# Kernel optimization log

Hardware: AMD Instinct MI355X
Metric: run time of the kernel (lower is better)

Reference implementation:

```python
import jax, jax.numpy as jnp
import numpy as np

ROPE_BASE = 10000.0

def rope_2d(x, h, w):
    # x: (b, h, w, c); 2D RoPE, first half of pair-channels rotated by row angle, second by col angle
    b, _, _, c = x.shape
    k_max = c // 4  # c // (2 * num_spatial_dims)
    theta = 1.0 / (ROPE_BASE ** (jnp.arange(k_max, dtype=jnp.float32) / k_max))  # (k_max,)
    ang_h = jnp.arange(h, dtype=jnp.float32)[:, None] * theta  # (h, k_max)
    ang_w = jnp.arange(w, dtype=jnp.float32)[:, None] * theta  # (w, k_max)
    # angles: (h, w, 2*k_max) = cat([i*theta, j*theta], -1)
    angles = jnp.concatenate([
        jnp.broadcast_to(ang_h[:, None, :], (h, w, k_max)),
        jnp.broadcast_to(ang_w[None, :, :], (h, w, k_max)),
    ], axis=-1)
    cos = jnp.cos(angles)  # (h, w, c//2)
    sin = jnp.sin(angles)
    xr = x[..., 0::2]  # consecutive-pair real parts (b,h,w,c//2)
    xi = x[..., 1::2]
    out_r = xr * cos - xi * sin
    out_i = xr * sin + xi * cos
    return jnp.stack([out_r, out_i], axis=-1).reshape(b, h, w, c)

def linear_attention_fwd(x, h, w, qk_w, qk_b, lepe_w, lepe_b, num_heads=4):
    b, n, c = x.shape
    head_dim = c // num_heads
    qk = x @ qk_w.T + qk_b  # (b, n, 2c)
    q, k = qk[..., :c], qk[..., c:]
    v = x
    q = jax.nn.elu(q) + 1.0
    k = jax.nn.elu(k) + 1.0
    q_rope = rope_2d(q.reshape(b, h, w, c), h, w).reshape(b, n, num_heads, head_dim).transpose(0, 2, 1, 3)
    k_rope = rope_2d(k.reshape(b, h, w, c), h, w).reshape(b, n, num_heads, head_dim).transpose(0, 2, 1, 3)
    qh = q.reshape(b, n, num_heads, head_dim).transpose(0, 2, 1, 3)  # (b,H,n,d)
    kh = k.reshape(b, n, num_heads, head_dim).transpose(0, 2, 1, 3)
    vh = v.reshape(b, n, num_heads, head_dim).transpose(0, 2, 1, 3)
    k_mean = kh.mean(axis=2)  # (b,H,d)
    z = 1.0 / (jnp.einsum('bhnd,bhd->bhn', qh, k_mean) + 1e-6)  # (b,H,n)
    inv_n = 1.0 / n
    kv = jnp.einsum('bhnd,bhne->bhde', k_rope, vh) * inv_n  # (b,H,d,d)
    out = jnp.einsum('bhnd,bhde->bhne', q_rope, kv) * z[..., None]  # (b,H,n,d)
    out = out.transpose(0, 2, 1, 3).reshape(b, n, c)
    # LePE: depthwise 3x3 conv on v in NCHW
    v_img = v.reshape(b, h, w, c).transpose(0, 3, 1, 2)  # (b,c,h,w)
    lepe = jax.lax.conv_general_dilated(
        v_img, lepe_w, window_strides=(1, 1), padding='SAME',
        feature_group_count=c, dimension_numbers=('NCHW', 'OIHW', 'NCHW'))
    lepe = lepe + lepe_b[None, :, None, None]
    out = out + lepe.transpose(0, 2, 3, 1).reshape(b, n, c)
    return out.transpose(0, 2, 1).reshape(b, c, h, w)

def setup_inputs() -> dict:
    key = jax.random.key(0)
    ks = jax.random.split(key, 5)
    b, h, w, c = 16, 128, 128, 64
    n = h * w
    x = jax.random.normal(ks[0], (b, n, c), dtype=jnp.float32)
    qk_w = jax.random.normal(ks[1], (2 * c, c), dtype=jnp.float32) * (1.0 / np.sqrt(c))
    qk_b = jax.random.normal(ks[2], (2 * c,), dtype=jnp.float32) * 0.02
    lepe_w = jax.random.normal(ks[3], (c, 1, 3, 3), dtype=jnp.float32) * (1.0 / 3.0)
    lepe_b = jax.random.normal(ks[4], (c,), dtype=jnp.float32) * 0.02
    return {"x": x, "h": h, "w": w, "qk_w": qk_w, "qk_b": qk_b, "lepe_w": lepe_w, "lepe_b": lepe_b}

def reference(x, h, w, qk_w, qk_b, lepe_w, lepe_b):
    return linear_attention_fwd(x, h, w, qk_w, qk_b, lepe_w, lepe_b, num_heads=4)
```

## Files before the change

kernel.cpp:

```cpp
#include <hip/hip_runtime.h>

#define B_   16
#define C_   64
#define HH   128
#define WW   128
#define NN   (HH*WW)
#define PADB 72
#define PADO 66

typedef short short8 __attribute__((ext_vector_type(8)));
typedef float f32x4  __attribute__((ext_vector_type(4)));

#define NEG_L2_10K_OVER16 (-0.8304820237218406f)

__device__ __forceinline__ float act_elu1(float v) {
    return v > 0.f ? v + 1.f : __expf(v);
}
__device__ __forceinline__ short f2bf(float f) {
    union { float f; unsigned u; } v; v.f = f;
    unsigned r = (v.u + 0x7FFFu + ((v.u >> 16) & 1u)) >> 16;
    return (short)r;
}
__device__ __forceinline__ unsigned cvt2bf(float lo, float hi) {
    unsigned r;
    asm("v_cvt_pk_bf16_f32 %0, %1, %2" : "=v"(r) : "v"(lo), "v"(hi));
    return r;
}

__device__ __forceinline__ void p1_chunk(
    const float* __restrict__ xb, int n0, int xbase, const short8 bk[2][4],
    const float* biasK, const float* sy, const float* cy, const float* th,
    int w, int ln, int quad, short* sKTb, float* kmacc)
{
    short8 aF[2];
    #pragma unroll
    for (int ks = 0; ks < 2; ++ks) {
        const float* ap = xb + (size_t)(n0 + 16*w + ln)*C_ + 32*ks + 8*quad;
        float4 a0 = *(const float4*)ap, a1 = *(const float4*)(ap + 4);
        union { unsigned u[4]; short8 s; } af;
        af.u[0] = cvt2bf(a0.x, a0.y); af.u[1] = cvt2bf(a0.z, a0.w);
        af.u[2] = cvt2bf(a1.x, a1.y); af.u[3] = cvt2bf(a1.z, a1.w);
        aF[ks] = af.s;
    }
    f32x4 ak[4];
    #pragma unroll
    for (int nt = 0; nt < 4; ++nt) ak[nt] = (f32x4){0.f,0.f,0.f,0.f};
    #pragma unroll
    for (int ks = 0; ks < 2; ++ks)
        #pragma unroll
        for (int nt = 0; nt < 4; ++nt)
            ak[nt] = __builtin_amdgcn_mfma_f32_16x16x32_bf16(aF[ks], bk[ks][nt], ak[nt], 0, 0, 0);
    const int p_base = 16*w + 4*quad;
    #pragma unroll
    for (int nt = 0; nt < 4; ++nt) {
        const int j = 16*nt + ln;
        const float sgn = (j & 1) ? 1.f : -1.f;
        #pragma unroll
        for (int r = 0; r < 4; ++r) {
            int p_loc = p_base + r;
            float kval = act_elu1(ak[nt][r] + biasK[nt]);
            kmacc[nt] += kval;
            float P = __shfl_xor(kval, 1);
            float s, c;
            if (nt < 2) { s = sy[nt]; c = cy[nt]; }
            else __sincosf((float)(xbase + p_loc) * th[nt & 1], &s, &c);
            sKTb[j*PADB + p_loc] = f2bf(kval*c + sgn*P*s);
        }
    }
}

__device__ __forceinline__ void p1_kv(
    const short* sKTb, const short* sXTb, int w, int ln, int quad, f32x4* acc2)
{
    #pragma unroll
    for (int ks = 0; ks < 2; ++ks) {
        short8 a  = *(const short8*)(sKTb + (16*w + ln)*PADB + 32*ks + 8*quad);
        short8 bf = *(const short8*)(sXTb + (16*w + ln)*PADB + 32*ks + 8*quad);
        *acc2 = __builtin_amdgcn_mfma_f32_16x16x32_bf16(a, bf, *acc2, 0, 0, 0);
    }
}

__global__ __launch_bounds__(256, 4) void la_phase1(
    const float* __restrict__ x, const float* __restrict__ qk_w,
    const float* __restrict__ qk_b, float* __restrict__ g_kv,
    float* __restrict__ g_km)
{
    __shared__ __align__(16) char pool[4*64*PADB*2 + 256*4];
    short* sXT0 = (short*)pool;
    short* sKT0 = sXT0 + 64*PADB;
    short* sXT1 = sKT0 + 64*PADB;
    short* sKT1 = sXT1 + 64*PADB;
    float* kmp  = (float*)(sKT1 + 64*PADB);

    const int tid  = threadIdx.x;
    const int w    = tid >> 6;
    const int ln   = tid & 15;
    const int quad = (tid >> 4) & 3;
    const int b    = blockIdx.y;
    const int bx   = blockIdx.x;
    const int nblk = ((bx & 7) << 4) | (bx >> 3);
    const float* xb = x + (size_t)b * (size_t)(NN * C_);

    short8 bk[2][4];
    #pragma unroll
    for (int ks = 0; ks < 2; ++ks)
        #pragma unroll
        for (int nt = 0; nt < 4; ++nt) {
            const float* wp = qk_w + (64 + 16*nt + ln)*C_ + 32*ks + 8*quad;
            float4 w0 = *(const float4*)wp, w1 = *(const float4*)(wp + 4);
            union { unsigned u[4]; short8 s; } uf;
            uf.u[0] = cvt2bf(w0.x, w0.y); uf.u[1] = cvt2bf(w0.z, w0.w);
            uf.u[2] = cvt2bf(w1.x, w1.y); uf.u[3] = cvt2bf(w1.z, w1.w);
            bk[ks][nt] = uf.s;
        }
    float biasK[4];
    #pragma unroll
    for (int nt = 0; nt < 4; ++nt) biasK[nt] = qk_b[64 + 16*nt + ln];

    float th[2];
    #pragma unroll
    for (int i = 0; i < 2; ++i)
        th[i] = exp2f(NEG_L2_10K_OVER16 * (float)(8*i + (ln >> 1)));
    float sy[2], cy[2];
    #pragma unroll
    for (int i = 0; i < 2; ++i) __sincosf((float)nblk * th[i], &sy[i], &cy[i]);

    const int srow = tid & 63, scol = (tid >> 6) << 2;
    float4 xv0[4], xv1[4];
    #pragma unroll
    for (int it = 0; it < 4; ++it)
        xv0[it] = *(const float4*)(xb + (size_t)(nblk*128 + srow)*C_ + scol + 16*it);
    #pragma unroll
    for (int it = 0; it < 4; ++it) {
        int k4 = scol + 16*it;
        unsigned p01 = cvt2bf(xv0[it].x, xv0[it].y), p23 = cvt2bf(xv0[it].z, xv0[it].w);
        sXT0[(k4+0)*PADB + srow] = (short)p01;
        sXT0[(k4+1)*PADB + srow] = (short)(p01 >> 16);
        sXT0[(k4+2)*PADB + srow] = (short)p23;
        sXT0[(k4+3)*PADB + srow] = (short)(p23 >> 16);
    }
    #pragma unroll
    for (int it = 0; it < 4; ++it)
        xv1[it] = *(const float4*)(xb + (size_t)(nblk*128 + 64 + srow)*C_ + scol + 16*it);
    __syncthreads();

    f32x4 acc2 = {0.f, 0.f, 0.f, 0.f};
    float kmacc[4] = {0.f, 0.f, 0.f, 0.f};

    p1_chunk(xb, nblk*128, 0, bk, biasK, sy, cy, th, w, ln, quad, sKT0, kmacc);
    #pragma unroll
    for (int it = 0; it < 4; ++it) {
        int k4 = scol + 16*it;
        unsigned p01 = cvt2bf(xv1[it].x, xv1[it].y), p23 = cvt2bf(xv1[it].z, xv1[it].w);
        sXT1[(k4+0)*PADB + srow] = (short)p01;
        sXT1[(k4+1)*PADB + srow] = (short)(p01 >> 16);
        sXT1[(k4+2)*PADB + srow] = (short)p23;
        sXT1[(k4+3)*PADB + srow] = (short)(p23 >> 16);
    }
    __syncthreads();
    p1_kv(sKT0, sXT0, w, ln, quad, &acc2);
    p1_chunk(xb, nblk*128 + 64, 64, bk, biasK, sy, cy, th, w, ln, quad, sKT1, kmacc);
    __syncthreads();
    p1_kv(sKT1, sXT1, w, ln, quad, &acc2);

    float* kvb = g_kv + b*1024;
    #pragma unroll
    for (int r = 0; r < 4; ++r)
        atomicAdd(kvb + w*256 + (4*quad + r)*16 + ln, acc2[r]);

    #pragma unroll
    for (int nt = 0; nt < 4; ++nt) {
        float v = kmacc[nt];
        v += __shfl_xor(v, 16);
        v += __shfl_xor(v, 32);
        if ((tid & 63) < 16) kmp[w*64 + 16*nt + ln] = v;
    }
    __syncthreads();
    if (tid < 64)
        atomicAdd(g_km + b*64 + tid,
                  kmp[tid] + kmp[64 + tid] + kmp[128 + tid] + kmp[192 + tid]);
}

__global__ __launch_bounds__(256, 8) void la_phase2(
    const float* __restrict__ x, const float* __restrict__ qk_w,
    const float* __restrict__ qk_b, const float* __restrict__ lepe_w,
    const float* __restrict__ lepe_b, const float* __restrict__ g_kv,
    const float* __restrict__ g_km, float* __restrict__ out)
{
    __shared__ __align__(16) char pool[16896 + 2304];
    short* sKVB = (short*)pool;
    short* sQ   = (short*)(pool + 5120);
    float* sOut = (float*)pool;
    float* sWT  = (float*)(pool + 16896);

    const int tid  = threadIdx.x;
    const int w    = tid >> 6;
    const int ln   = tid & 15;
    const int quad = (tid >> 4) & 3;
    const int b    = blockIdx.y;
    const int bx   = blockIdx.x;
    const int n0   = (((bx & 7) << 5) | (bx >> 3)) * 64;
    const float* xb = x + (size_t)b * (size_t)(NN * C_);
    const float inv_n = 1.f / (float)NN;

    for (int idx = tid; idx < 1024; idx += 256) {
        int h = idx >> 8, d = (idx >> 4) & 15, e = idx & 15;
        float v = g_kv[b*1024 + idx] * inv_n;
        int rowb = h*16 + e;
        int kpos  = (h & 1) ? 16 + d : d;
        int kzero = (h & 1) ? d : 16 + d;
        sKVB[rowb*40 + kpos]  = f2bf(v);
        sKVB[rowb*40 + kzero] = 0;
    }
    if (tid < 144) {
        float4 lw = *(const float4*)(lepe_w + tid*4);
        float lwv[4] = {lw.x, lw.y, lw.z, lw.w};
        #pragma unroll
        for (int i = 0; i < 4; ++i) {
            int e = tid*4 + i, ch = e / 9, tap = e - ch*9;
            sWT[tap*64 + ch] = lwv[i];
        }
    }

    short8 wq[2][4];
    #pragma unroll
    for (int ks = 0; ks < 2; ++ks)
        #pragma unroll
        for (int nt = 0; nt < 4; ++nt) {
            const float* wp = qk_w + (16*nt + ln)*C_ + 32*ks + 8*quad;
            float4 w0 = *(const float4*)wp, w1 = *(const float4*)(wp + 4);
            union { unsigned u[4]; short8 s; } uf;
            uf.u[0] = cvt2bf(w0.x, w0.y); uf.u[1] = cvt2bf(w0.z, w0.w);
            uf.u[2] = cvt2bf(w1.x, w1.y); uf.u[3] = cvt2bf(w1.z, w1.w);
            wq[ks][nt] = uf.s;
        }
    float biasq[4], kmv[4];
    #pragma unroll
    for (int nt = 0; nt < 4; ++nt) {
        biasq[nt] = qk_b[16*nt + ln];
        kmv[nt]   = g_km[b*64 + 16*nt + ln];
    }
    short8 aF[2];
    #pragma unroll
    for (int ks = 0; ks < 2; ++ks) {
        const float* ap = xb + (size_t)(n0 + 16*w + ln)*C_ + 32*ks + 8*quad;
        float4 a0 = *(const float4*)ap, a1 = *(const float4*)(ap + 4);
        union { unsigned u[4]; short8 s; } af;
        af.u[0] = cvt2bf(a0.x, a0.y);
        af.u[1] = cvt2bf(a0.z, a0.w);
        af.u[2] = cvt2bf(a1.x, a1.y);
        af.u[3] = cvt2bf(a1.z, a1.w);
        aF[ks] = af.s;
    }
    f32x4 aq[4];
    #pragma unroll
    for (int nt = 0; nt < 4; ++nt) aq[nt] = (f32x4){0.f,0.f,0.f,0.f};
    #pragma unroll
    for (int ks = 0; ks < 2; ++ks)
        #pragma unroll
        for (int nt = 0; nt < 4; ++nt)
            aq[nt] = __builtin_amdgcn_mfma_f32_16x16x32_bf16(aF[ks], wq[ks][nt], aq[nt], 0, 0, 0);

    float qv[4][4];
    #pragma unroll
    for (int nt = 0; nt < 4; ++nt)
        #pragma unroll
        for (int r = 0; r < 4; ++r) {
            float q0 = act_elu1(aq[nt][r] + biasq[nt]);
            float dp = q0 * kmv[nt];
            dp += __shfl_xor(dp, 1);
            dp += __shfl_xor(dp, 2);
            dp += __shfl_xor(dp, 4);
            dp += __shfl_xor(dp, 8);
            qv[nt][r] = q0 / (dp * inv_n + 1e-6f);
        }

    float th[2];
    #pragma unroll
    for (int i = 0; i < 2; ++i)
        th[i] = exp2f(NEG_L2_10K_OVER16 * (float)(8*i + (ln >> 1)));
    const int ycoord = n0 >> 7;
    const int x0 = n0 & 127;
    float sy[2], cy[2];
    #pragma unroll
    for (int i = 0; i < 2; ++i) __sincosf((float)ycoord * th[i], &sy[i], &cy[i]);
    const int p_base = 16*w + 4*quad;
    #pragma unroll
    for (int nt = 0; nt < 4; ++nt) {
        const int j = 16*nt + ln;
        const float sgn = (j & 1) ? 1.f : -1.f;
        #pragma unroll
        for (int r = 0; r < 4; ++r) {
            int p_loc = p_base + r;
            float s, c;
            if (nt < 2) { s = sy[nt]; c = cy[nt]; }
            else __sincosf((float)(x0 + p_loc) * th[nt & 1], &s, &c);
            float P = __shfl_xor(qv[nt][r], 1);
            sQ[p_loc*PADB + j] = f2bf(qv[nt][r]*c + sgn*P*s);
        }
    }
    __syncthreads();

    f32x4 accq[4];
    #pragma unroll
    for (int h = 0; h < 4; ++h) accq[h] = (f32x4){0.f,0.f,0.f,0.f};
    #pragma unroll
    for (int P2 = 0; P2 < 2; ++P2) {
        short8 a = *(const short8*)(sQ + (16*w + ln)*PADB + 32*P2 + 8*quad);
        #pragma unroll
        for (int hh = 0; hh < 2; ++hh) {
            int h = 2*P2 + hh;
            short8 bf = *(const short8*)(sKVB + (h*16 + ln)*40 + 8*quad);
            accq[h] = __builtin_amdgcn_mfma_f32_16x16x32_bf16(a, bf, accq[h], 0, 0, 0);
        }
    }
    __syncthreads();

    #pragma unroll
    for (int h = 0; h < 4; ++h)
        #pragma unroll
        for (int r = 0; r < 4; ++r)
            sOut[(16*h + ln)*PADO + 16*w + 4*quad + r] = accq[h][r];

    const int cg = tid & 15;
    const int pg = tid >> 4;
    const int p0 = 4*pg;
    const int yy = n0 >> 7, xbase = n0 & 127, gx0 = xbase + p0;
    f32x4 accl[4];
    #pragma unroll
    for (int j = 0; j < 4; ++j) accl[j] = (f32x4){0.f,0.f,0.f,0.f};
    #pragma unroll
    for (int dy = -1; dy <= 1; ++dy) {
        int y2 = yy + dy;
        if ((unsigned)y2 >= HH) continue;
        f32x4 wt0 = *(const f32x4*)(sWT + ((dy+1)*3 + 0)*C_ + 4*cg);
        f32x4 wt1 = *(const f32x4*)(sWT + ((dy+1)*3 + 1)*C_ + 4*cg);
        f32x4 wt2 = *(const f32x4*)(sWT + ((dy+1)*3 + 2)*C_ + 4*cg);
        const float* rp = xb + (size_t)(y2*WW)*C_ + 4*cg;
        f32x4 cb[6];
        #pragma unroll
        for (int jj = 0; jj < 6; ++jj) {
            int col = gx0 - 1 + jj;
            cb[jj] = ((unsigned)col < WW) ? *(const f32x4*)(rp + (size_t)col*C_)
                                          : (f32x4){0.f,0.f,0.f,0.f};
        }
        #pragma unroll
        for (int j = 0; j < 4; ++j)
            accl[j] += cb[j]*wt0 + cb[j+1]*wt1 + cb[j+2]*wt2;
    }
    __syncthreads();
    #pragma unroll
    for (int j = 0; j < 4; ++j)
        #pragma unroll
        for (int i = 0; i < 4; ++i)
            sOut[(4*cg + i)*PADO + p0 + j] += accl[j][i];
    __syncthreads();

    const int ch = tid >> 2, sub = tid & 3, pp0 = 16*sub;
    const float lb = lepe_b[ch];
    float* outp = out + (size_t)b*(size_t)(C_*NN) + (size_t)ch*NN + n0 + pp0;
    #pragma unroll
    for (int g = 0; g < 4; ++g) {
        float2 a0 = *(const float2*)(sOut + ch*PADO + pp0 + 4*g);
        float2 a1 = *(const float2*)(sOut + ch*PADO + pp0 + 4*g + 2);
        float4 o4 = { a0.x + lb, a0.y + lb, a1.x + lb, a1.y + lb };
        *(float4*)(outp + 4*g) = o4;
    }
}

extern "C" void kernel_launch(void* const* d_in, const int* in_sizes, int n_in,
                              void* d_out, int out_size, void* d_ws, size_t ws_size,
                              hipStream_t stream) {
    const float* x      = (const float*)d_in[0];
    const float* qk_w   = (const float*)d_in[3];
    const float* qk_b   = (const float*)d_in[4];
    const float* lepe_w = (const float*)d_in[5];
    const float* lepe_b = (const float*)d_in[6];
    float* out = (float*)d_out;

    float* g_kv = (float*)d_ws;
    float* g_km = g_kv + 16*1024;
    hipMemsetAsync(d_ws, 0, (size_t)(16*1024 + 16*64) * sizeof(float), stream);

    hipLaunchKernelGGL(la_phase1, dim3(128, B_), dim3(256), 0, stream,
                       x, qk_w, qk_b, g_kv, g_km);
    hipLaunchKernelGGL(la_phase2, dim3(256, B_), dim3(256), 0, stream,
                       x, qk_w, qk_b, lepe_w, lepe_b, g_kv, g_km, out);
}
```

Measured before the change: 202.5 us.

## Process four chunks per phase-1 block with double-buffered loads and rotation recurrence

Phase 1 now handles 256 positions per block instead of 128, halving the grid. It loops over four 64-row chunks with register-prefetched x and ping-pong shared buffers. This halves the number of global atomics on kv and k_mean and overlaps loads with compute. Both phases replace per-element sincos for column angles with one sincos plus an angle-addition recurrence, and phase 2 swaps a division for a hardware reciprocal. The risks are fewer blocks in flight for phase 1 and small accumulated rounding error from the recurrence.

```diff
diff --git a/kernel.cpp b/kernel.cpp
--- a/kernel.cpp
+++ b/kernel.cpp
@@ -27,70 +27,13 @@
     return r;
 }
 
-__device__ __forceinline__ void p1_chunk(
-    const float* __restrict__ xb, int n0, int xbase, const short8 bk[2][4],
-    const float* biasK, const float* sy, const float* cy, const float* th,
-    int w, int ln, int quad, short* sKTb, float* kmacc)
-{
-    short8 aF[2];
-    #pragma unroll
-    for (int ks = 0; ks < 2; ++ks) {
-        const float* ap = xb + (size_t)(n0 + 16*w + ln)*C_ + 32*ks + 8*quad;
-        float4 a0 = *(const float4*)ap, a1 = *(const float4*)(ap + 4);
-        union { unsigned u[4]; short8 s; } af;
-        af.u[0] = cvt2bf(a0.x, a0.y); af.u[1] = cvt2bf(a0.z, a0.w);
-        af.u[2] = cvt2bf(a1.x, a1.y); af.u[3] = cvt2bf(a1.z, a1.w);
-        aF[ks] = af.s;
-    }
-    f32x4 ak[4];
-    #pragma unroll
-    for (int nt = 0; nt < 4; ++nt) ak[nt] = (f32x4){0.f,0.f,0.f,0.f};
-    #pragma unroll
-    for (int ks = 0; ks < 2; ++ks)
-        #pragma unroll
-        for (int nt = 0; nt < 4; ++nt)
-            ak[nt] = __builtin_amdgcn_mfma_f32_16x16x32_bf16(aF[ks], bk[ks][nt], ak[nt], 0, 0, 0);
-    const int p_base = 16*w + 4*quad;
-    #pragma unroll
-    for (int nt = 0; nt < 4; ++nt) {
-        const int j = 16*nt + ln;
-        const float sgn = (j & 1) ? 1.f : -1.f;
-        #pragma unroll
-        for (int r = 0; r < 4; ++r) {
-            int p_loc = p_base + r;
-            float kval = act_elu1(ak[nt][r] + biasK[nt]);
-            kmacc[nt] += kval;
-            float P = __shfl_xor(kval, 1);
-            float s, c;
-            if (nt < 2) { s = sy[nt]; c = cy[nt]; }
-            else __sincosf((float)(xbase + p_loc) * th[nt & 1], &s, &c);
-            sKTb[j*PADB + p_loc] = f2bf(kval*c + sgn*P*s);
-        }
-    }
-}
-
-__device__ __forceinline__ void p1_kv(
-    const short* sKTb, const short* sXTb, int w, int ln, int quad, f32x4* acc2)
-{
-    #pragma unroll
-    for (int ks = 0; ks < 2; ++ks) {
-        short8 a  = *(const short8*)(sKTb + (16*w + ln)*PADB + 32*ks + 8*quad);
-        short8 bf = *(const short8*)(sXTb + (16*w + ln)*PADB + 32*ks + 8*quad);
-        *acc2 = __builtin_amdgcn_mfma_f32_16x16x32_bf16(a, bf, *acc2, 0, 0, 0);
-    }
-}
-
 __global__ __launch_bounds__(256, 4) void la_phase1(
     const float* __restrict__ x, const float* __restrict__ qk_w,
     const float* __restrict__ qk_b, float* __restrict__ g_kv,
     float* __restrict__ g_km)
 {
     __shared__ __align__(16) char pool[4*64*PADB*2 + 256*4];
-    short* sXT0 = (short*)pool;
-    short* sKT0 = sXT0 + 64*PADB;
-    short* sXT1 = sKT0 + 64*PADB;
-    short* sKT1 = sXT1 + 64*PADB;
-    float* kmp  = (float*)(sKT1 + 64*PADB);
+    float* kmp = (float*)(pool + 36864);
 
     const int tid  = threadIdx.x;
     const int w    = tid >> 6;
@@ -98,8 +41,15 @@
     const int quad = (tid >> 4) & 3;
     const int b    = blockIdx.y;
     const int bx   = blockIdx.x;
-    const int nblk = ((bx & 7) << 4) | (bx >> 3);
+    const int nid  = ((bx & 7) << 3) | (bx >> 3);
+    const int n_base = nid * 256;
     const float* xb = x + (size_t)b * (size_t)(NN * C_);
+
+    const int srow = tid & 63, scol = (tid >> 6) << 2;
+    f32x4 xv[2][4];
+    #pragma unroll
+    for (int it = 0; it < 4; ++it)
+        xv[0][it] = *(const f32x4*)(xb + (size_t)(n_base + srow)*C_ + scol + 16*it);
 
     short8 bk[2][4];
     #pragma unroll
@@ -107,67 +57,110 @@
         #pragma unroll
         for (int nt = 0; nt < 4; ++nt) {
             const float* wp = qk_w + (64 + 16*nt + ln)*C_ + 32*ks + 8*quad;
-            float4 w0 = *(const float4*)wp, w1 = *(const float4*)(wp + 4);
+            f32x4 w0 = *(const f32x4*)wp, w1 = *(const f32x4*)(wp + 4);
             union { unsigned u[4]; short8 s; } uf;
-            uf.u[0] = cvt2bf(w0.x, w0.y); uf.u[1] = cvt2bf(w0.z, w0.w);
-            uf.u[2] = cvt2bf(w1.x, w1.y); uf.u[3] = cvt2bf(w1.z, w1.w);
+            uf.u[0] = cvt2bf(w0[0], w0[1]); uf.u[1] = cvt2bf(w0[2], w0[3]);
+            uf.u[2] = cvt2bf(w1[0], w1[1]); uf.u[3] = cvt2bf(w1[2], w1[3]);
             bk[ks][nt] = uf.s;
         }
     float biasK[4];
     #pragma unroll
     for (int nt = 0; nt < 4; ++nt) biasK[nt] = qk_b[64 + 16*nt + ln];
 
-    float th[2];
-    #pragma unroll
-    for (int i = 0; i < 2; ++i)
+    float th[2], rs[2], rc[2];
+    #pragma unroll
+    for (int i = 0; i < 2; ++i) {
         th[i] = exp2f(NEG_L2_10K_OVER16 * (float)(8*i + (ln >> 1)));
-    float sy[2], cy[2];
-    #pragma unroll
-    for (int i = 0; i < 2; ++i) __sincosf((float)nblk * th[i], &sy[i], &cy[i]);
-
-    const int srow = tid & 63, scol = (tid >> 6) << 2;
-    float4 xv0[4], xv1[4];
-    #pragma unroll
-    for (int it = 0; it < 4; ++it)
-        xv0[it] = *(const float4*)(xb + (size_t)(nblk*128 + srow)*C_ + scol + 16*it);
-    #pragma unroll
-    for (int it = 0; it < 4; ++it) {
-        int k4 = scol + 16*it;
-        unsigned p01 = cvt2bf(xv0[it].x, xv0[it].y), p23 = cvt2bf(xv0[it].z, xv0[it].w);
-        sXT0[(k4+0)*PADB + srow] = (short)p01;
-        sXT0[(k4+1)*PADB + srow] = (short)(p01 >> 16);
-        sXT0[(k4+2)*PADB + srow] = (short)p23;
-        sXT0[(k4+3)*PADB + srow] = (short)(p23 >> 16);
-    }
-    #pragma unroll
-    for (int it = 0; it < 4; ++it)
-        xv1[it] = *(const float4*)(xb + (size_t)(nblk*128 + 64 + srow)*C_ + scol + 16*it);
-    __syncthreads();
+        __sincosf(th[i], &rs[i], &rc[i]);
+    }
 
     f32x4 acc2 = {0.f, 0.f, 0.f, 0.f};
     float kmacc[4] = {0.f, 0.f, 0.f, 0.f};
-
-    p1_chunk(xb, nblk*128, 0, bk, biasK, sy, cy, th, w, ln, quad, sKT0, kmacc);
-    #pragma unroll
-    for (int it = 0; it < 4; ++it) {
-        int k4 = scol + 16*it;
-        unsigned p01 = cvt2bf(xv1[it].x, xv1[it].y), p23 = cvt2bf(xv1[it].z, xv1[it].w);
-        sXT1[(k4+0)*PADB + srow] = (short)p01;
-        sXT1[(k4+1)*PADB + srow] = (short)(p01 >> 16);
-        sXT1[(k4+2)*PADB + srow] = (short)p23;
-        sXT1[(k4+3)*PADB + srow] = (short)(p23 >> 16);
-    }
-    __syncthreads();
-    p1_kv(sKT0, sXT0, w, ln, quad, &acc2);
-    p1_chunk(xb, nblk*128 + 64, 64, bk, biasK, sy, cy, th, w, ln, quad, sKT1, kmacc);
-    __syncthreads();
-    p1_kv(sKT1, sXT1, w, ln, quad, &acc2);
+    const int p_base = 16*w + 4*quad;
+    const float sgn = (ln & 1) ? 1.f : -1.f;
+
+    #pragma unroll
+    for (int ck = 0; ck < 4; ++ck) {
+        const int cur = ck & 1;
+        const int n0  = n_base + ck*64;
+        short* sXT = (short*)(pool + cur*18432);
+        short* sKT = (short*)(pool + cur*18432 + 9216);
+        __syncthreads();
+        #pragma unroll
+        for (int it = 0; it < 4; ++it) {
+            int k4 = scol + 16*it;
+            unsigned p01 = cvt2bf(xv[cur][it][0], xv[cur][it][1]);
+            unsigned p23 = cvt2bf(xv[cur][it][2], xv[cur][it][3]);
+            sXT[(k4+0)*PADB + srow] = (short)p01;
+            sXT[(k4+1)*PADB + srow] = (short)(p01 >> 16);
+            sXT[(k4+2)*PADB + srow] = (short)p23;
+            sXT[(k4+3)*PADB + srow] = (short)(p23 >> 16);
+        }
+        if (ck < 3) {
+            #pragma unroll
+            for (int it = 0; it < 4; ++it)
+                xv[cur^1][it] = *(const f32x4*)(xb + (size_t)(n0 + 64 + srow)*C_ + scol + 16*it);
+        }
+        short8 aF[2];
+        const float* ap = xb + (size_t)(n0 + 16*w + ln)*C_;
+        #pragma unroll
+        for (int ks = 0; ks < 2; ++ks) {
+            f32x4 a0 = *(const f32x4*)(ap + 32*ks + 8*quad);
+            f32x4 a1 = *(const f32x4*)(ap + 32*ks + 8*quad + 4);
+            union { unsigned u[4]; short8 s; } af;
+            af.u[0] = cvt2bf(a0[0], a0[1]); af.u[1] = cvt2bf(a0[2], a0[3]);
+            af.u[2] = cvt2bf(a1[0], a1[1]); af.u[3] = cvt2bf(a1[2], a1[3]);
+            aF[ks] = af.s;
+        }
+        f32x4 ak[4];
+        #pragma unroll
+        for (int nt = 0; nt < 4; ++nt) ak[nt] = (f32x4){0.f,0.f,0.f,0.f};
+        #pragma unroll
+        for (int ks = 0; ks < 2; ++ks)
+            #pragma unroll
+            for (int nt = 0; nt < 4; ++nt)
+                ak[nt] = __builtin_amdgcn_mfma_f32_16x16x32_bf16(aF[ks], bk[ks][nt], ak[nt], 0, 0, 0);
+
+        const int yc = n0 >> 7;
+        const int x0 = n0 & 127;
+        float sy[2], cy[2];
+        #pragma unroll
+        for (int i = 0; i < 2; ++i) __sincosf((float)yc * th[i], &sy[i], &cy[i]);
+        #pragma unroll
+        for (int nt = 0; nt < 4; ++nt) {
+            float xs = 0.f, xc = 1.f;
+            if (nt >= 2)
+                __sincosf((float)(x0 + p_base) * th[nt & 1], &xs, &xc);
+            #pragma unroll
+            for (int r = 0; r < 4; ++r) {
+                int p_loc = p_base + r;
+                float kval = act_elu1(ak[nt][r] + biasK[nt]);
+                kmacc[nt] += kval;
+                float P = __shfl_xor(kval, 1);
+                float s, c;
+                if (nt < 2) { s = sy[nt]; c = cy[nt]; }
+                else {
+                    s = xs; c = xc;
+                    float ns = xs*rc[nt & 1] + xc*rs[nt & 1];
+                    float nc = xc*rc[nt & 1] - xs*rs[nt & 1];
+                    xs = ns; xc = nc;
+                }
+                sKT[(16*nt + ln)*PADB + p_loc] = f2bf(kval*c + sgn*P*s);
+            }
+        }
+        __syncthreads();
+        #pragma unroll
+        for (int ks = 0; ks < 2; ++ks) {
+            short8 a  = *(const short8*)(sKT + (16*w + ln)*PADB + 32*ks + 8*quad);
+            short8 bf = *(const short8*)(sXT + (16*w + ln)*PADB + 32*ks + 8*quad);
+            acc2 = __builtin_amdgcn_mfma_f32_16x16x32_bf16(a, bf, acc2, 0, 0, 0);
+        }
+    }
 
     float* kvb = g_kv + b*1024;
     #pragma unroll
     for (int r = 0; r < 4; ++r)
         atomicAdd(kvb + w*256 + (4*quad + r)*16 + ln, acc2[r]);
-
     #pragma unroll
     for (int nt = 0; nt < 4; ++nt) {
         float v = kmacc[nt];
@@ -228,10 +221,10 @@
         #pragma unroll
         for (int nt = 0; nt < 4; ++nt) {
             const float* wp = qk_w + (16*nt + ln)*C_ + 32*ks + 8*quad;
-            float4 w0 = *(const float4*)wp, w1 = *(const float4*)(wp + 4);
+            f32x4 w0 = *(const f32x4*)wp, w1 = *(const f32x4*)(wp + 4);
             union { unsigned u[4]; short8 s; } uf;
-            uf.u[0] = cvt2bf(w0.x, w0.y); uf.u[1] = cvt2bf(w0.z, w0.w);
-            uf.u[2] = cvt2bf(w1.x, w1.y); uf.u[3] = cvt2bf(w1.z, w1.w);
+            uf.u[0] = cvt2bf(w0[0], w0[1]); uf.u[1] = cvt2bf(w0[2], w0[3]);
+            uf.u[2] = cvt2bf(w1[0], w1[1]); uf.u[3] = cvt2bf(w1[2], w1[3]);
             wq[ks][nt] = uf.s;
         }
     float biasq[4], kmv[4];
@@ -244,12 +237,12 @@
     #pragma unroll
     for (int ks = 0; ks < 2; ++ks) {
         const float* ap = xb + (size_t)(n0 + 16*w + ln)*C_ + 32*ks + 8*quad;
-        float4 a0 = *(const float4*)ap, a1 = *(const float4*)(ap + 4);
+        f32x4 a0 = *(const f32x4*)ap, a1 = *(const f32x4*)(ap + 4);
         union { unsigned u[4]; short8 s; } af;
-        af.u[0] = cvt2bf(a0.x, a0.y);
-        af.u[1] = cvt2bf(a0.z, a0.w);
-        af.u[2] = cvt2bf(a1.x, a1.y);
-        af.u[3] = cvt2bf(a1.z, a1.w);
+        af.u[0] = cvt2bf(a0[0], a0[1]);
+        af.u[1] = cvt2bf(a0[2], a0[3]);
+        af.u[2] = cvt2bf(a1[0], a1[1]);
+        af.u[3] = cvt2bf(a1[2], a1[3]);
         aF[ks] = af.s;
     }
     f32x4 aq[4];
@@ -272,31 +265,40 @@
             dp += __shfl_xor(dp, 2);
             dp += __shfl_xor(dp, 4);
             dp += __shfl_xor(dp, 8);
-            qv[nt][r] = q0 / (dp * inv_n + 1e-6f);
-        }
-
-    float th[2];
-    #pragma unroll
-    for (int i = 0; i < 2; ++i)
+            qv[nt][r] = q0 * __builtin_amdgcn_rcpf(dp * inv_n + 1e-6f);
+        }
+
+    float th[2], rs[2], rc[2];
+    #pragma unroll
+    for (int i = 0; i < 2; ++i) {
         th[i] = exp2f(NEG_L2_10K_OVER16 * (float)(8*i + (ln >> 1)));
+        __sincosf(th[i], &rs[i], &rc[i]);
+    }
     const int ycoord = n0 >> 7;
     const int x0 = n0 & 127;
     float sy[2], cy[2];
     #pragma unroll
     for (int i = 0; i < 2; ++i) __sincosf((float)ycoord * th[i], &sy[i], &cy[i]);
     const int p_base = 16*w + 4*quad;
+    const float sgn = (ln & 1) ? 1.f : -1.f;
     #pragma unroll
     for (int nt = 0; nt < 4; ++nt) {
-        const int j = 16*nt + ln;
-        const float sgn = (j & 1) ? 1.f : -1.f;
+        float xs = 0.f, xc = 1.f;
+        if (nt >= 2)
+            __sincosf((float)(x0 + p_base) * th[nt & 1], &xs, &xc);
         #pragma unroll
         for (int r = 0; r < 4; ++r) {
             int p_loc = p_base + r;
             float s, c;
             if (nt < 2) { s = sy[nt]; c = cy[nt]; }
-            else __sincosf((float)(x0 + p_loc) * th[nt & 1], &s, &c);
+            else {
+                s = xs; c = xc;
+                float ns = xs*rc[nt & 1] + xc*rs[nt & 1];
+                float nc = xc*rc[nt & 1] - xs*rs[nt & 1];
+                xs = ns; xc = nc;
+            }
             float P = __shfl_xor(qv[nt][r], 1);
-            sQ[p_loc*PADB + j] = f2bf(qv[nt][r]*c + sgn*P*s);
+            sQ[p_loc*PADB + (16*nt + ln)] = f2bf(qv[nt][r]*c + sgn*P*s);
         }
     }
     __syncthreads();
@@ -320,7 +322,7 @@
     for (int h = 0; h < 4; ++h)
         #pragma unroll
         for (int r = 0; r < 4; ++r)
-            sOut[(16*h + ln)*PADO + 16*w + 4*quad + r] = accq[h][r];
+            sOut[(16*h + ln)*PADO + p_base + r] = accq[h][r];
 
     const int cg = tid & 15;
     const int pg = tid >> 4;
@@ -382,7 +384,7 @@
     float* g_km = g_kv + 16*1024;
     hipMemsetAsync(d_ws, 0, (size_t)(16*1024 + 16*64) * sizeof(float), stream);
 
-    hipLaunchKernelGGL(la_phase1, dim3(128, B_), dim3(256), 0, stream,
+    hipLaunchKernelGGL(la_phase1, dim3(64, B_), dim3(256), 0, stream,
                        x, qk_w, qk_b, g_kv, g_km);
     hipLaunchKernelGGL(la_phase2, dim3(256, B_), dim3(256), 0, stream,
                        x, qk_w, qk_b, lepe_w, lepe_b, g_kv, g_km, out);
```

Measured after the change: 214.7 us. 1.06x slower.
